# Optimization experiments

Hardware: AMD Instinct MI355X
Metric: run time of the kernel (lower is better)

## Reference

```python
import jax, jax.numpy as jnp
import numpy as np

DIM_IN, DIM_OUT, DIM_CTX = 128, 256, 259
B, N, S_CTX = 32, 2048, 1
BN_EPS = 1e-5


def setup_inputs() -> dict:
    key = jax.random.key(0)
    ks = jax.random.split(key, 12)
    s = 0.02
    return {
        "ctx": jax.random.normal(ks[0], (B, S_CTX, DIM_CTX), jnp.float32),
        "x": jax.random.normal(ks[1], (B, N, DIM_IN), jnp.float32),
        "W_layer": jax.random.normal(ks[2], (DIM_OUT, DIM_IN), jnp.float32) * s,
        "b_layer": jax.random.normal(ks[3], (DIM_OUT,), jnp.float32) * s,
        "W_hbias": jax.random.normal(ks[4], (DIM_OUT, DIM_CTX), jnp.float32) * s,
        "W_gate": jax.random.normal(ks[5], (DIM_OUT, DIM_CTX), jnp.float32) * s,
        "b_gate": jax.random.normal(ks[6], (DIM_OUT,), jnp.float32) * s,
        "W_k": jax.random.normal(ks[7], (DIM_OUT, DIM_CTX - 3), jnp.float32) * s,
        "W_v": jax.random.normal(ks[8], (DIM_OUT, DIM_CTX - 3), jnp.float32) * s,
        "W_tc": jax.random.normal(ks[9], (DIM_OUT, DIM_OUT), jnp.float32) * s,
        "b_tc": jax.random.normal(ks[10], (DIM_OUT,), jnp.float32) * s,
        "bn_gamma": jnp.ones((N,), jnp.float32),
        "bn_beta": jnp.zeros((N,), jnp.float32),
    }


def reference(ctx, x, W_layer, b_layer, W_hbias, W_gate, b_gate, W_k, W_v, W_tc, b_tc, bn_gamma, bn_beta):
    # FiLM gate / bias from context: [B, 1, dim_out]
    gate = jax.nn.sigmoid(jnp.einsum('bsc,oc->bso', ctx, W_gate) + b_gate)
    bias = jnp.einsum('bsc,oc->bso', ctx, W_hbias)

    # main linear: [B, N, dim_out]
    x1 = jnp.einsum('bni,oi->bno', x, W_layer) + b_layer

    # channel attention from shape context (drop last 3 ctx dims)
    shape = ctx[:, :, : ctx.shape[2] - 3]                      # [B, S, C-3]
    shape_k = jnp.einsum('bsc,oc->bos', shape, W_k)            # [B, dim_out, S]
    shape_v = jnp.einsum('bsc,oc->bso', shape, W_v)            # [B, S, dim_out]
    energy = jnp.einsum('bos,bse->boe', shape_k, shape_v)      # [B, dim_out, dim_out]
    attention = jax.nn.softmax(energy, axis=-1)
    attention = attention / (1e-9 + attention.sum(axis=1, keepdims=True))

    # channel mixing: [B, N, dim_out]
    x_r = jnp.einsum('bno,boe->bne', x1, attention)

    # trans_conv + BatchNorm1d(N) (train-mode batch stats over dims (0, 2)) + ReLU
    t = jnp.einsum('bno,eo->bne', x1 - x_r, W_tc) + b_tc       # [B, N, dim_out]
    mean = t.mean(axis=(0, 2), keepdims=True)                  # per point-channel
    var = t.var(axis=(0, 2), keepdims=True)                    # biased variance
    t = (t - mean) * jax.lax.rsqrt(var + BN_EPS)
    t = t * bn_gamma[None, :, None] + bn_beta[None, :, None]
    x_r = jax.nn.relu(t)

    xo = x1 + x_r
    return xo * gate + bias
```

## Files before the change

kernel.cpp:

```cpp
#include <hip/hip_runtime.h>
#include <hip/hip_bf16.h>

#define BB   32
#define NN   2048
#define DIN  128
#define DOUT 256
#define DCTX 259

#define OFF_TT   0u
#define OFF_AB   0u
#define OFF_MTB  1048576u
#define OFF_X1B  8388608u
#define OFF_WMB  16777216u
#define OFF_WLB  17301504u
#define OFF_WLTB 17317888u
#define OFF_WTCB 17334272u
#define OFF_G    17367040u
#define OFF_HB   17375232u
#define OFF_TB   17383424u
#define OFF_WKT  17391616u
#define OFF_WVT  17457152u
#define OFF_WGT  17522688u
#define OFF_WHT  17588992u

typedef short bf16x8 __attribute__((ext_vector_type(8)));
typedef float f32x4  __attribute__((ext_vector_type(4)));

static __device__ inline unsigned short f2bf(float f) {
    __hip_bfloat16 h = __float2bfloat16(f);
    return *(unsigned short*)&h;
}
static __device__ inline float bf2f(unsigned short u) {
    unsigned v = ((unsigned)u) << 16;
    float f;
    __builtin_memcpy(&f, &v, 4);
    return f;
}

__global__ void kXW(const float* __restrict__ Wl, const float* __restrict__ Wtc,
                    const float* __restrict__ Wk, const float* __restrict__ Wv,
                    const float* __restrict__ Wg, const float* __restrict__ Whb,
                    float* __restrict__ ws) {
    unsigned bb = blockIdx.x, t = threadIdx.x;
    if (bb < 8u) {
        unsigned base = bb * 8192u;
        unsigned short* dst = (unsigned short*)(ws + OFF_WTCB);
#pragma unroll
        for (int j = 0; j < 32; j++) {
            unsigned i = base + (unsigned)j * 256u + t;
            dst[i] = f2bf(Wtc[i]);
        }
    } else if (bb == 8u) {
        unsigned short* dst = (unsigned short*)(ws + OFF_WLTB);
        for (unsigned idx = t; idx < 32768u; idx += 256u) {
            unsigned i = idx >> 8, o = idx & 255u;
            dst[idx] = f2bf(Wl[o * 128u + i]);
        }
    } else if (bb == 9u) {
        unsigned short* dst = (unsigned short*)(ws + OFF_WLB);
        for (unsigned idx = t; idx < 32768u; idx += 256u) dst[idx] = f2bf(Wl[idx]);
    } else {
        unsigned j = bb - 10u;
        const float* src; float* dst; unsigned C, c0;
        if (j < 8u)       { src = Wk;  dst = ws + OFF_WKT; C = 256; c0 = j * 32u; }
        else if (j < 16u) { src = Wv;  dst = ws + OFF_WVT; C = 256; c0 = (j - 8u) * 32u; }
        else if (j < 25u) { src = Wg;  dst = ws + OFF_WGT; C = 259; c0 = (j - 16u) * 32u; }
        else              { src = Whb; dst = ws + OFF_WHT; C = 259; c0 = (j - 25u) * 32u; }
        for (unsigned cc = c0; cc < c0 + 32u && cc < C; cc++)
            dst[cc * 256u + t] = src[t * C + cc];
    }
}

__global__ __launch_bounds__(1024) void kP(const float* __restrict__ ctx,
                                           const float* __restrict__ bg,
                                           float* __restrict__ ws) {
    const int b = blockIdx.x, t = threadIdx.x;
    const int o = t & 255, q = t >> 8;
    __shared__ __align__(16) float cs[260];
    __shared__ __align__(16) float ks[256], vs[256], rms[256], ris[256];
    __shared__ float pm[1024], ps[1024];
    for (int i = t; i < DCTX; i += 1024) cs[i] = ctx[b * DCTX + i];
    __syncthreads();

    {
        const float* WT; int C;
        if (q == 0)      { WT = ws + OFF_WKT; C = 256; }
        else if (q == 1) { WT = ws + OFF_WVT; C = 256; }
        else if (q == 2) { WT = ws + OFF_WGT; C = DCTX; }
        else             { WT = ws + OFF_WHT; C = DCTX; }
        float s = 0.f;
#pragma unroll 8
        for (int c = 0; c < C; c++) s += WT[c * 256 + o] * cs[c];
        if (q == 0)      ks[o] = s;
        else if (q == 1) vs[o] = s;
        else if (q == 2) ws[OFF_G + b * DOUT + o] = 1.f / (1.f + __expf(-(s + bg[o])));
        else             ws[OFF_HB + b * DOUT + o] = s;
    }
    __syncthreads();

    const float ko = ks[o];
    const float4* vs4 = (const float4*)vs;
    float pmax = -1e30f;
#pragma unroll 4
    for (int j = q * 16; j < q * 16 + 16; j++) {
        float4 v = vs4[j];
        pmax = fmaxf(pmax, fmaxf(fmaxf(ko * v.x, ko * v.y), fmaxf(ko * v.z, ko * v.w)));
    }
    pm[q * 256 + o] = pmax;
    __syncthreads();
    float m = fmaxf(fmaxf(pm[o], pm[256 + o]), fmaxf(pm[512 + o], pm[768 + o]));
    float psum = 0.f;
#pragma unroll 4
    for (int j = q * 16; j < q * 16 + 16; j++) {
        float4 v = vs4[j];
        psum += __expf(ko * v.x - m) + __expf(ko * v.y - m)
              + __expf(ko * v.z - m) + __expf(ko * v.w - m);
    }
    ps[q * 256 + o] = psum;
    __syncthreads();
    float ri = 1.f / (ps[o] + ps[256 + o] + ps[512 + o] + ps[768 + o]);
    if (q == 0) { rms[o] = m; ris[o] = ri; }
    __syncthreads();

    const float ve = vs[o];
    float cp = 0.f;
#pragma unroll 4
    for (int o2 = q * 64; o2 < q * 64 + 64; o2++)
        cp += __expf(ks[o2] * ve - rms[o2]) * ris[o2];
    pm[q * 256 + o] = cp;
    __syncthreads();
    float ci = 1.f / (1e-9f + pm[o] + pm[256 + o] + pm[512 + o] + pm[768 + o]);
    unsigned short* Ab = (unsigned short*)(ws + OFF_AB) + (size_t)b * 65536u;
#pragma unroll 4
    for (int o2 = q * 64; o2 < q * 64 + 64; o2++) {
        float a = __expf(ks[o2] * ve - rms[o2]) * ris[o2] * ci;
        Ab[o2 * 256 + o] = f2bf(a);
    }
}

__global__ __launch_bounds__(256) void k4m(float* __restrict__ ws) {
    const int t = threadIdx.x, wid = t >> 6, l = t & 63;
    const int b = blockIdx.y, et = blockIdx.x;
    const int lrow = l & 15, lk = l >> 4;
    const int rbase = et * 64 + (wid & 1) * 32;
    const int colbase = (wid >> 1) * 128;
    const unsigned short* Wtcb = (const unsigned short*)(ws + OFF_WTCB);
    const unsigned short* Ab = (const unsigned short*)(ws + OFF_AB) + (size_t)b * 65536u;

    f32x4 acc[2][8];
#pragma unroll
    for (int i = 0; i < 2; i++)
#pragma unroll
        for (int c = 0; c < 8; c++) acc[i][c] = (f32x4){0.f, 0.f, 0.f, 0.f};

    const unsigned short* ar0 = Wtcb + (rbase + lrow) * 256;
#pragma unroll
    for (int kk = 0; kk < 8; kk++) {
        int ko = kk * 32 + lk * 8;
        bf16x8 a0 = *(const bf16x8*)(ar0 + ko);
        bf16x8 a1 = *(const bf16x8*)(ar0 + 16 * 256 + ko);
        bf16x8 bfr[8];
#pragma unroll
        for (int c = 0; c < 8; c++)
            bfr[c] = *(const bf16x8*)(Ab + (colbase + c * 16 + lrow) * 256 + ko);
#pragma unroll
        for (int c = 0; c < 8; c++) {
            acc[0][c] = __builtin_amdgcn_mfma_f32_16x16x32_bf16(a0, bfr[c], acc[0][c], 0, 0, 0);
            acc[1][c] = __builtin_amdgcn_mfma_f32_16x16x32_bf16(a1, bfr[c], acc[1][c], 0, 0, 0);
        }
    }
    unsigned short* Mtb = (unsigned short*)(ws + OFF_MTB) + (size_t)b * 65536u;
#pragma unroll
    for (int t2 = 0; t2 < 2; t2++)
#pragma unroll
        for (int c = 0; c < 8; c++)
#pragma unroll
            for (int r = 0; r < 4; r++) {
                int row = rbase + t2 * 16 + lk * 4 + r;
                int col = colbase + c * 16 + lrow;
                float idv = bf2f(Wtcb[row * 256 + col]);
                Mtb[row * 256 + col] = f2bf(idv - acc[t2][c][r]);
            }
}

__global__ __launch_bounds__(256) void k5m(const float* __restrict__ bl,
                                           const float* __restrict__ btc,
                                           float* __restrict__ ws) {
    const int t = threadIdx.x, wid = t >> 6, l = t & 63;
    const int b = blockIdx.y, et = blockIdx.x;
    const int lrow = l & 15, lk = l >> 4;
    const int rbase = et * 128 + wid * 32;
    const unsigned short* Mtb = (const unsigned short*)(ws + OFF_MTB) + (size_t)b * 65536u;
    const unsigned short* Wltb = (const unsigned short*)(ws + OFF_WLTB);

    f32x4 acc[2][8];
#pragma unroll
    for (int i = 0; i < 2; i++)
#pragma unroll
        for (int c = 0; c < 8; c++) acc[i][c] = (f32x4){0.f, 0.f, 0.f, 0.f};

    const unsigned short* ar0 = Mtb + (rbase + lrow) * 256;
#pragma unroll
    for (int kk = 0; kk < 8; kk++) {
        int ko = kk * 32 + lk * 8;
        bf16x8 a0 = *(const bf16x8*)(ar0 + ko);
        bf16x8 a1 = *(const bf16x8*)(ar0 + 16 * 256 + ko);
        bf16x8 bfr[8];
#pragma unroll
        for (int c = 0; c < 8; c++)
            bfr[c] = *(const bf16x8*)(Wltb + (c * 16 + lrow) * 256 + ko);
#pragma unroll
        for (int c = 0; c < 8; c++) {
            acc[0][c] = __builtin_amdgcn_mfma_f32_16x16x32_bf16(a0, bfr[c], acc[0][c], 0, 0, 0);
            acc[1][c] = __builtin_amdgcn_mfma_f32_16x16x32_bf16(a1, bfr[c], acc[1][c], 0, 0, 0);
        }
    }
    unsigned short* WMBp = (unsigned short*)(ws + OFF_WMB) + (size_t)b * 32768u;
#pragma unroll
    for (int t2 = 0; t2 < 2; t2++)
#pragma unroll
        for (int c = 0; c < 8; c++)
#pragma unroll
            for (int r = 0; r < 4; r++) {
                int row = rbase + t2 * 16 + lk * 4 + r;
                int col = c * 16 + lrow;
                WMBp[row * 128 + col] = f2bf(acc[t2][c][r]);
            }
    if (t < 128) {
        int e = et * 128 + t;
        const unsigned short* mrow = Mtb + e * 256;
        float s = 0.f;
#pragma unroll 8
        for (int o = 0; o < 256; o++) s += bl[o] * bf2f(mrow[o]);
        ws[OFF_TB + b * DOUT + e] = s + btc[e];
    }
}

#define LDP 136
__global__ __launch_bounds__(256) void k6_mfma(const float* __restrict__ x,
                                               const float* __restrict__ bl,
                                               float* __restrict__ ws) {
    const int t = threadIdx.x;
    const int wid = t >> 6, l = t & 63;
    const int b = blockIdx.y;
    const int n0 = blockIdx.x * 64;
    const int lrow = l & 15, lk = l >> 4;
    __shared__ unsigned short xs[64 * LDP];

    const float4* xg = (const float4*)(x + (size_t)(b * NN + n0) * DIN);
#pragma unroll
    for (int it = 0; it < 8; it++) {
        int idx = it * 256 + t;
        int row = idx >> 5, kq = idx & 31;
        float4 v = xg[idx];
        ushort4 u;
        u.x = f2bf(v.x); u.y = f2bf(v.y); u.z = f2bf(v.z); u.w = f2bf(v.w);
        *(ushort4*)(xs + row * LDP + kq * 4) = u;
    }
    __syncthreads();

    unsigned short* x1p = (unsigned short*)(ws + OFF_X1B);
    unsigned short* ttp = (unsigned short*)(ws + OFF_TT);
    const int colbase = wid * 64;

#pragma unroll
    for (int tc = 0; tc < 2; tc++) {
        const unsigned short* wb = (tc == 0)
            ? (const unsigned short*)(ws + OFF_WLB)
            : (const unsigned short*)(ws + OFF_WMB) + (size_t)b * 32768u;
        float bias[4];
#pragma unroll
        for (int ct = 0; ct < 4; ct++) {
            int col = colbase + ct * 16 + lrow;
            bias[ct] = (tc == 0) ? bl[col] : ws[OFF_TB + b * DOUT + col];
        }
        f32x4 acc[4][4];
#pragma unroll
        for (int rt = 0; rt < 4; rt++)
#pragma unroll
            for (int ct = 0; ct < 4; ct++) acc[rt][ct] = (f32x4){0.f, 0.f, 0.f, 0.f};

#pragma unroll
        for (int kk = 0; kk < 4; kk++) {
            int ko = kk * 32 + lk * 8;
            bf16x8 a[4];
#pragma unroll
            for (int rt = 0; rt < 4; rt++)
                a[rt] = *(const bf16x8*)(xs + (rt * 16 + lrow) * LDP + ko);
            bf16x8 bf[4];
#pragma unroll
            for (int ct = 0; ct < 4; ct++)
                bf[ct] = *(const bf16x8*)(wb + (size_t)(colbase + ct * 16 + lrow) * DIN + ko);
#pragma unroll
            for (int rt = 0; rt < 4; rt++)
#pragma unroll
                for (int ct = 0; ct < 4; ct++)
                    acc[rt][ct] = __builtin_amdgcn_mfma_f32_16x16x32_bf16(a[rt], bf[ct], acc[rt][ct], 0, 0, 0);
        }
        unsigned short* dst = (tc == 0) ? x1p : ttp;
#pragma unroll
        for (int rt = 0; rt < 4; rt++)
#pragma unroll
            for (int ct = 0; ct < 4; ct++)
#pragma unroll
                for (int r = 0; r < 4; r++) {
                    int row = n0 + rt * 16 + lk * 4 + r;
                    int col = colbase + ct * 16 + lrow;
                    dst[(size_t)((b * NN + row) * DOUT) + col] = f2bf(acc[rt][ct][r] + bias[ct]);
                }
    }
}

__global__ __launch_bounds__(1024) void k78(const float* __restrict__ gamma,
                                            const float* __restrict__ beta,
                                            float* __restrict__ out,
                                            float* __restrict__ ws) {
    const int n = blockIdx.x, t = threadIdx.x;
    const int o = t & 255, q = t >> 8;
    const int wid = t >> 6, l = t & 63;
    const unsigned short* ttb = (const unsigned short*)(ws + OFF_TT);
    const unsigned short* x1b = (const unsigned short*)(ws + OFF_X1B);
    float v[8];
    float s1 = 0.f, s2 = 0.f;
#pragma unroll
    for (int j = 0; j < 8; j++) {
        int b = q * 8 + j;
        float vv = bf2f(ttb[((size_t)b * NN + n) * DOUT + o]);
        v[j] = vv; s1 += vv; s2 += vv * vv;
    }
#pragma unroll
    for (int off = 32; off > 0; off >>= 1) {
        s1 += __shfl_xor(s1, off, 64);
        s2 += __shfl_xor(s2, off, 64);
    }
    __shared__ float p1[16], p2[16];
    if (l == 0) { p1[wid] = s1; p2[wid] = s2; }
    __syncthreads();
    float S1 = 0.f, S2 = 0.f;
#pragma unroll
    for (int w = 0; w < 16; w++) { S1 += p1[w]; S2 += p2[w]; }
    float mean = S1 * (1.f / 8192.f);
    float var  = S2 * (1.f / 8192.f) - mean * mean;
    float sc = gamma[n] * rsqrtf(fmaxf(var, 0.f) + 1e-5f);
    float sh = beta[n] - mean * sc;
#pragma unroll
    for (int j = 0; j < 8; j++) {
        int b = q * 8 + j;
        float x1 = bf2f(x1b[((size_t)b * NN + n) * DOUT + o]);
        float g  = ws[OFF_G  + b * DOUT + o];
        float hb = ws[OFF_HB + b * DOUT + o];
        out[((size_t)b * NN + n) * DOUT + o] = (x1 + fmaxf(v[j] * sc + sh, 0.f)) * g + hb;
    }
}

extern "C" void kernel_launch(void* const* d_in, const int* in_sizes, int n_in,
                              void* d_out, int out_size, void* d_ws, size_t ws_size,
                              hipStream_t stream) {
    const float* ctx   = (const float*)d_in[0];
    const float* x     = (const float*)d_in[1];
    const float* Wl    = (const float*)d_in[2];
    const float* bl    = (const float*)d_in[3];
    const float* Whb   = (const float*)d_in[4];
    const float* Wg    = (const float*)d_in[5];
    const float* bg    = (const float*)d_in[6];
    const float* Wk    = (const float*)d_in[7];
    const float* Wv    = (const float*)d_in[8];
    const float* Wtc   = (const float*)d_in[9];
    const float* btc   = (const float*)d_in[10];
    const float* gamma = (const float*)d_in[11];
    const float* beta  = (const float*)d_in[12];
    float* out = (float*)d_out;
    float* ws  = (float*)d_ws;

    kXW     <<<44, 256, 0, stream>>>(Wl, Wtc, Wk, Wv, Wg, Whb, ws);
    kP      <<<BB, 1024, 0, stream>>>(ctx, bg, ws);
    k4m     <<<dim3(4, BB), 256, 0, stream>>>(ws);
    k5m     <<<dim3(2, BB), 256, 0, stream>>>(bl, btc, ws);
    k6_mfma <<<dim3(32, BB), 256, 0, stream>>>(x, bl, ws);
    k78     <<<NN, 1024, 0, stream>>>(gamma, beta, out, ws);
}
```

Before: 240.4 us.

## Fuse the BN statistics pass into the GEMM with atomics and a per-tile spin barrier

Merges k4m and k5m into one kernel that keeps the intermediate M matrix in swizzled LDS rather than global memory. Merges the x1/t GEMM kernel with the BatchNorm+ReLU+FiLM epilogue. Per-point batch statistics are reduced with atomics, and the 32 batch blocks of each n-tile synchronise on a spin counter. This removes the bf16 t tensor round trip through HBM and two kernel launches. In exchange it needs all 1024 blocks to be co-resident, otherwise the spin barrier deadlocks, and atomic ordering makes the float sums nondeterministic.

```diff
diff --git a/kernel.cpp b/kernel.cpp
--- a/kernel.cpp
+++ b/kernel.cpp
@@ -9,7 +9,6 @@
 
 #define OFF_TT   0u
 #define OFF_AB   0u
-#define OFF_MTB  1048576u
 #define OFF_X1B  8388608u
 #define OFF_WMB  16777216u
 #define OFF_WLB  17301504u
@@ -22,6 +21,8 @@
 #define OFF_WVT  17457152u
 #define OFF_WGT  17522688u
 #define OFF_WHT  17588992u
+#define OFF_STATS 17655296u
+#define OFF_CNT   17659392u
 
 typedef short bf16x8 __attribute__((ext_vector_type(8)));
 typedef float f32x4  __attribute__((ext_vector_type(4)));
@@ -59,6 +60,8 @@
     } else if (bb == 9u) {
         unsigned short* dst = (unsigned short*)(ws + OFF_WLB);
         for (unsigned idx = t; idx < 32768u; idx += 256u) dst[idx] = f2bf(Wl[idx]);
+    } else if (bb == 44u) {
+        for (unsigned i = t; i < 4128u; i += 256u) ws[OFF_STATS + i] = 0.f;
     } else {
         unsigned j = bb - 10u;
         const float* src; float* dst; unsigned C, c0;
@@ -138,114 +141,115 @@
     }
 }
 
-__global__ __launch_bounds__(256) void k4m(float* __restrict__ ws) {
-    const int t = threadIdx.x, wid = t >> 6, l = t & 63;
-    const int b = blockIdx.y, et = blockIdx.x;
-    const int lrow = l & 15, lk = l >> 4;
-    const int rbase = et * 64 + (wid & 1) * 32;
-    const int colbase = (wid >> 1) * 128;
-    const unsigned short* Wtcb = (const unsigned short*)(ws + OFF_WTCB);
-    const unsigned short* Ab = (const unsigned short*)(ws + OFF_AB) + (size_t)b * 65536u;
-
-    f32x4 acc[2][8];
-#pragma unroll
-    for (int i = 0; i < 2; i++)
-#pragma unroll
-        for (int c = 0; c < 8; c++) acc[i][c] = (f32x4){0.f, 0.f, 0.f, 0.f};
-
-    const unsigned short* ar0 = Wtcb + (rbase + lrow) * 256;
-#pragma unroll
-    for (int kk = 0; kk < 8; kk++) {
-        int ko = kk * 32 + lk * 8;
-        bf16x8 a0 = *(const bf16x8*)(ar0 + ko);
-        bf16x8 a1 = *(const bf16x8*)(ar0 + 16 * 256 + ko);
-        bf16x8 bfr[8];
-#pragma unroll
-        for (int c = 0; c < 8; c++)
-            bfr[c] = *(const bf16x8*)(Ab + (colbase + c * 16 + lrow) * 256 + ko);
-#pragma unroll
-        for (int c = 0; c < 8; c++) {
-            acc[0][c] = __builtin_amdgcn_mfma_f32_16x16x32_bf16(a0, bfr[c], acc[0][c], 0, 0, 0);
-            acc[1][c] = __builtin_amdgcn_mfma_f32_16x16x32_bf16(a1, bfr[c], acc[1][c], 0, 0, 0);
-        }
-    }
-    unsigned short* Mtb = (unsigned short*)(ws + OFF_MTB) + (size_t)b * 65536u;
-#pragma unroll
-    for (int t2 = 0; t2 < 2; t2++)
-#pragma unroll
-        for (int c = 0; c < 8; c++)
-#pragma unroll
-            for (int r = 0; r < 4; r++) {
-                int row = rbase + t2 * 16 + lk * 4 + r;
-                int col = colbase + c * 16 + lrow;
-                float idv = bf2f(Wtcb[row * 256 + col]);
-                Mtb[row * 256 + col] = f2bf(idv - acc[t2][c][r]);
-            }
-}
-
-__global__ __launch_bounds__(256) void k5m(const float* __restrict__ bl,
+__global__ __launch_bounds__(512) void k45(const float* __restrict__ bl,
                                            const float* __restrict__ btc,
                                            float* __restrict__ ws) {
     const int t = threadIdx.x, wid = t >> 6, l = t & 63;
     const int b = blockIdx.y, et = blockIdx.x;
     const int lrow = l & 15, lk = l >> 4;
-    const int rbase = et * 128 + wid * 32;
-    const unsigned short* Mtb = (const unsigned short*)(ws + OFF_MTB) + (size_t)b * 65536u;
-    const unsigned short* Wltb = (const unsigned short*)(ws + OFF_WLTB);
-
-    f32x4 acc[2][8];
-#pragma unroll
-    for (int i = 0; i < 2; i++)
-#pragma unroll
-        for (int c = 0; c < 8; c++) acc[i][c] = (f32x4){0.f, 0.f, 0.f, 0.f};
-
-    const unsigned short* ar0 = Mtb + (rbase + lrow) * 256;
-#pragma unroll
-    for (int kk = 0; kk < 8; kk++) {
-        int ko = kk * 32 + lk * 8;
-        bf16x8 a0 = *(const bf16x8*)(ar0 + ko);
-        bf16x8 a1 = *(const bf16x8*)(ar0 + 16 * 256 + ko);
-        bf16x8 bfr[8];
+    __shared__ unsigned short Mt[128 * 256];
+    const unsigned short* Wtcb = (const unsigned short*)(ws + OFF_WTCB);
+
+    {
+        const unsigned short* Ab = (const unsigned short*)(ws + OFF_AB) + (size_t)b * 65536u;
+        const int sub = wid >> 2, w2 = wid & 3;
+        const int rbase = et * 128 + sub * 64 + (w2 & 1) * 32;
+        const int colbase = (w2 >> 1) * 128;
+        f32x4 acc[2][8];
+#pragma unroll
+        for (int i = 0; i < 2; i++)
+#pragma unroll
+            for (int c = 0; c < 8; c++) acc[i][c] = (f32x4){0.f, 0.f, 0.f, 0.f};
+        const unsigned short* ar0 = Wtcb + (rbase + lrow) * 256;
+#pragma unroll
+        for (int kk = 0; kk < 8; kk++) {
+            int ko = kk * 32 + lk * 8;
+            bf16x8 a0 = *(const bf16x8*)(ar0 + ko);
+            bf16x8 a1 = *(const bf16x8*)(ar0 + 16 * 256 + ko);
+            bf16x8 bfr[8];
+#pragma unroll
+            for (int c = 0; c < 8; c++)
+                bfr[c] = *(const bf16x8*)(Ab + (colbase + c * 16 + lrow) * 256 + ko);
+#pragma unroll
+            for (int c = 0; c < 8; c++) {
+                acc[0][c] = __builtin_amdgcn_mfma_f32_16x16x32_bf16(a0, bfr[c], acc[0][c], 0, 0, 0);
+                acc[1][c] = __builtin_amdgcn_mfma_f32_16x16x32_bf16(a1, bfr[c], acc[1][c], 0, 0, 0);
+            }
+        }
+#pragma unroll
+        for (int t2 = 0; t2 < 2; t2++)
+#pragma unroll
+            for (int c = 0; c < 8; c++)
+#pragma unroll
+                for (int r = 0; r < 4; r++) {
+                    int grow = rbase + t2 * 16 + lk * 4 + r;
+                    int col = colbase + c * 16 + lrow;
+                    float idv = bf2f(Wtcb[grow * 256 + col]);
+                    int rl = grow - et * 128;
+                    Mt[rl * 256 + (col ^ ((rl & 7) << 3))] = f2bf(idv - acc[t2][c][r]);
+                }
+    }
+    __syncthreads();
+    {
+        const unsigned short* Wltb = (const unsigned short*)(ws + OFF_WLTB);
+        const int rl0 = wid * 16;
+        f32x4 acc[8];
+#pragma unroll
+        for (int c = 0; c < 8; c++) acc[c] = (f32x4){0.f, 0.f, 0.f, 0.f};
+        const int arow = rl0 + lrow;
+        const int asw = (arow & 7) << 3;
+#pragma unroll
+        for (int kk = 0; kk < 8; kk++) {
+            int ko = kk * 32 + lk * 8;
+            bf16x8 a0 = *(const bf16x8*)(Mt + arow * 256 + (ko ^ asw));
+            bf16x8 bfr[8];
+#pragma unroll
+            for (int c = 0; c < 8; c++)
+                bfr[c] = *(const bf16x8*)(Wltb + (c * 16 + lrow) * 256 + ko);
+#pragma unroll
+            for (int c = 0; c < 8; c++)
+                acc[c] = __builtin_amdgcn_mfma_f32_16x16x32_bf16(a0, bfr[c], acc[c], 0, 0, 0);
+        }
+        unsigned short* WMBp = (unsigned short*)(ws + OFF_WMB) + (size_t)b * 32768u;
 #pragma unroll
         for (int c = 0; c < 8; c++)
-            bfr[c] = *(const bf16x8*)(Wltb + (c * 16 + lrow) * 256 + ko);
-#pragma unroll
-        for (int c = 0; c < 8; c++) {
-            acc[0][c] = __builtin_amdgcn_mfma_f32_16x16x32_bf16(a0, bfr[c], acc[0][c], 0, 0, 0);
-            acc[1][c] = __builtin_amdgcn_mfma_f32_16x16x32_bf16(a1, bfr[c], acc[1][c], 0, 0, 0);
-        }
-    }
-    unsigned short* WMBp = (unsigned short*)(ws + OFF_WMB) + (size_t)b * 32768u;
-#pragma unroll
-    for (int t2 = 0; t2 < 2; t2++)
-#pragma unroll
-        for (int c = 0; c < 8; c++)
 #pragma unroll
             for (int r = 0; r < 4; r++) {
-                int row = rbase + t2 * 16 + lk * 4 + r;
+                int row = et * 128 + rl0 + lk * 4 + r;
                 int col = c * 16 + lrow;
-                WMBp[row * 128 + col] = f2bf(acc[t2][c][r]);
-            }
+                WMBp[row * 128 + col] = f2bf(acc[c][r]);
+            }
+    }
     if (t < 128) {
-        int e = et * 128 + t;
-        const unsigned short* mrow = Mtb + e * 256;
+        const int rl = t;
+        const int sw = (rl & 7) << 3;
         float s = 0.f;
-#pragma unroll 8
-        for (int o = 0; o < 256; o++) s += bl[o] * bf2f(mrow[o]);
-        ws[OFF_TB + b * DOUT + e] = s + btc[e];
+#pragma unroll 4
+        for (int j = 0; j < 32; j++) {
+            bf16x8 ch = *(const bf16x8*)(Mt + rl * 256 + ((j * 8) ^ sw));
+#pragma unroll
+            for (int u = 0; u < 8; u++) s += bl[j * 8 + u] * bf2f((unsigned short)ch[u]);
+        }
+        ws[OFF_TB + b * DOUT + et * 128 + rl] = s + btc[et * 128 + rl];
     }
 }
 
 #define LDP 136
-__global__ __launch_bounds__(256) void k6_mfma(const float* __restrict__ x,
-                                               const float* __restrict__ bl,
-                                               float* __restrict__ ws) {
+__global__ __launch_bounds__(256, 4) void kF(const float* __restrict__ x,
+                                             const float* __restrict__ bl,
+                                             const float* __restrict__ gamma,
+                                             const float* __restrict__ beta,
+                                             float* __restrict__ out,
+                                             float* __restrict__ ws) {
     const int t = threadIdx.x;
     const int wid = t >> 6, l = t & 63;
     const int b = blockIdx.y;
-    const int n0 = blockIdx.x * 64;
+    const int nt = blockIdx.x;
+    const int n0 = nt * 64;
     const int lrow = l & 15, lk = l >> 4;
     __shared__ unsigned short xs[64 * LDP];
+    __shared__ float sp1[4][64], sp2[4][64];
+    __shared__ float scs[64], shs[64];
 
     const float4* xg = (const float4*)(x + (size_t)(b * NN + n0) * DIN);
 #pragma unroll
@@ -259,27 +263,16 @@
     }
     __syncthreads();
 
+    const int colbase = wid * 64;
     unsigned short* x1p = (unsigned short*)(ws + OFF_X1B);
-    unsigned short* ttp = (unsigned short*)(ws + OFF_TT);
-    const int colbase = wid * 64;
-
-#pragma unroll
-    for (int tc = 0; tc < 2; tc++) {
-        const unsigned short* wb = (tc == 0)
-            ? (const unsigned short*)(ws + OFF_WLB)
-            : (const unsigned short*)(ws + OFF_WMB) + (size_t)b * 32768u;
-        float bias[4];
-#pragma unroll
-        for (int ct = 0; ct < 4; ct++) {
-            int col = colbase + ct * 16 + lrow;
-            bias[ct] = (tc == 0) ? bl[col] : ws[OFF_TB + b * DOUT + col];
-        }
-        f32x4 acc[4][4];
+
+    {
+        const unsigned short* wb = (const unsigned short*)(ws + OFF_WLB);
+        f32x4 acc0[4][4];
 #pragma unroll
         for (int rt = 0; rt < 4; rt++)
 #pragma unroll
-            for (int ct = 0; ct < 4; ct++) acc[rt][ct] = (f32x4){0.f, 0.f, 0.f, 0.f};
-
+            for (int ct = 0; ct < 4; ct++) acc0[rt][ct] = (f32x4){0.f, 0.f, 0.f, 0.f};
 #pragma unroll
         for (int kk = 0; kk < 4; kk++) {
             int ko = kk * 32 + lk * 8;
@@ -295,62 +288,139 @@
             for (int rt = 0; rt < 4; rt++)
 #pragma unroll
                 for (int ct = 0; ct < 4; ct++)
-                    acc[rt][ct] = __builtin_amdgcn_mfma_f32_16x16x32_bf16(a[rt], bf[ct], acc[rt][ct], 0, 0, 0);
-        }
-        unsigned short* dst = (tc == 0) ? x1p : ttp;
-#pragma unroll
-        for (int rt = 0; rt < 4; rt++)
-#pragma unroll
-            for (int ct = 0; ct < 4; ct++)
+                    acc0[rt][ct] = __builtin_amdgcn_mfma_f32_16x16x32_bf16(a[rt], bf[ct], acc0[rt][ct], 0, 0, 0);
+        }
+#pragma unroll
+        for (int ct = 0; ct < 4; ct++) {
+            float bv = bl[colbase + ct * 16 + lrow];
+#pragma unroll
+            for (int rt = 0; rt < 4; rt++)
 #pragma unroll
                 for (int r = 0; r < 4; r++) {
                     int row = n0 + rt * 16 + lk * 4 + r;
                     int col = colbase + ct * 16 + lrow;
-                    dst[(size_t)((b * NN + row) * DOUT) + col] = f2bf(acc[rt][ct][r] + bias[ct]);
+                    x1p[(size_t)((b * NN + row) * DOUT) + col] = f2bf(acc0[rt][ct][r] + bv);
                 }
-    }
-}
-
-__global__ __launch_bounds__(1024) void k78(const float* __restrict__ gamma,
-                                            const float* __restrict__ beta,
-                                            float* __restrict__ out,
-                                            float* __restrict__ ws) {
-    const int n = blockIdx.x, t = threadIdx.x;
-    const int o = t & 255, q = t >> 8;
-    const int wid = t >> 6, l = t & 63;
-    const unsigned short* ttb = (const unsigned short*)(ws + OFF_TT);
-    const unsigned short* x1b = (const unsigned short*)(ws + OFF_X1B);
-    float v[8];
-    float s1 = 0.f, s2 = 0.f;
-#pragma unroll
-    for (int j = 0; j < 8; j++) {
-        int b = q * 8 + j;
-        float vv = bf2f(ttb[((size_t)b * NN + n) * DOUT + o]);
-        v[j] = vv; s1 += vv; s2 += vv * vv;
-    }
-#pragma unroll
-    for (int off = 32; off > 0; off >>= 1) {
-        s1 += __shfl_xor(s1, off, 64);
-        s2 += __shfl_xor(s2, off, 64);
-    }
-    __shared__ float p1[16], p2[16];
-    if (l == 0) { p1[wid] = s1; p2[wid] = s2; }
-    __syncthreads();
-    float S1 = 0.f, S2 = 0.f;
-#pragma unroll
-    for (int w = 0; w < 16; w++) { S1 += p1[w]; S2 += p2[w]; }
-    float mean = S1 * (1.f / 8192.f);
-    float var  = S2 * (1.f / 8192.f) - mean * mean;
-    float sc = gamma[n] * rsqrtf(fmaxf(var, 0.f) + 1e-5f);
-    float sh = beta[n] - mean * sc;
-#pragma unroll
-    for (int j = 0; j < 8; j++) {
-        int b = q * 8 + j;
-        float x1 = bf2f(x1b[((size_t)b * NN + n) * DOUT + o]);
-        float g  = ws[OFF_G  + b * DOUT + o];
-        float hb = ws[OFF_HB + b * DOUT + o];
-        out[((size_t)b * NN + n) * DOUT + o] = (x1 + fmaxf(v[j] * sc + sh, 0.f)) * g + hb;
-    }
+        }
+    }
+
+    f32x4 acc[4][4];
+#pragma unroll
+    for (int rt = 0; rt < 4; rt++)
+#pragma unroll
+        for (int ct = 0; ct < 4; ct++) acc[rt][ct] = (f32x4){0.f, 0.f, 0.f, 0.f};
+    {
+        const unsigned short* wb = (const unsigned short*)(ws + OFF_WMB) + (size_t)b * 32768u;
+#pragma unroll
+        for (int kk = 0; kk < 4; kk++) {
+            int ko = kk * 32 + lk * 8;
+            bf16x8 a[4];
+#pragma unroll
+            for (int rt = 0; rt < 4; rt++)
+                a[rt] = *(const bf16x8*)(xs + (rt * 16 + lrow) * LDP + ko);
+            bf16x8 bf[4];
+#pragma unroll
+            for (int ct = 0; ct < 4; ct++)
+                bf[ct] = *(const bf16x8*)(wb + (size_t)(colbase + ct * 16 + lrow) * DIN + ko);
+#pragma unroll
+            for (int rt = 0; rt < 4; rt++)
+#pragma unroll
+                for (int ct = 0; ct < 4; ct++)
+                    acc[rt][ct] = __builtin_amdgcn_mfma_f32_16x16x32_bf16(a[rt], bf[ct], acc[rt][ct], 0, 0, 0);
+        }
+#pragma unroll
+        for (int ct = 0; ct < 4; ct++) {
+            float bv = ws[OFF_TB + b * DOUT + colbase + ct * 16 + lrow];
+#pragma unroll
+            for (int rt = 0; rt < 4; rt++)
+#pragma unroll
+                for (int r = 0; r < 4; r++) acc[rt][ct][r] += bv;
+        }
+    }
+
+    float s1[4][4], s2[4][4];
+#pragma unroll
+    for (int rt = 0; rt < 4; rt++)
+#pragma unroll
+        for (int r = 0; r < 4; r++) { s1[rt][r] = 0.f; s2[rt][r] = 0.f; }
+#pragma unroll
+    for (int rt = 0; rt < 4; rt++)
+#pragma unroll
+        for (int ct = 0; ct < 4; ct++)
+#pragma unroll
+            for (int r = 0; r < 4; r++) {
+                float v = acc[rt][ct][r];
+                s1[rt][r] += v; s2[rt][r] += v * v;
+            }
+#pragma unroll
+    for (int off = 1; off < 16; off <<= 1) {
+#pragma unroll
+        for (int rt = 0; rt < 4; rt++)
+#pragma unroll
+            for (int r = 0; r < 4; r++) {
+                s1[rt][r] += __shfl_xor(s1[rt][r], off, 64);
+                s2[rt][r] += __shfl_xor(s2[rt][r], off, 64);
+            }
+    }
+    if (lrow == 0) {
+#pragma unroll
+        for (int rt = 0; rt < 4; rt++)
+#pragma unroll
+            for (int r = 0; r < 4; r++) {
+                int nidx = rt * 16 + lk * 4 + r;
+                sp1[wid][nidx] = s1[rt][r];
+                sp2[wid][nidx] = s2[rt][r];
+            }
+    }
+    __syncthreads();
+    float* stats = ws + OFF_STATS;
+    if (t < 64) {
+        float S1 = sp1[0][t] + sp1[1][t] + sp1[2][t] + sp1[3][t];
+        float S2 = sp2[0][t] + sp2[1][t] + sp2[2][t] + sp2[3][t];
+        atomicAdd(stats + (size_t)(n0 + t) * 2, S1);
+        atomicAdd(stats + (size_t)(n0 + t) * 2 + 1, S2);
+    }
+    __syncthreads();
+
+    unsigned* cnt = (unsigned*)(ws + OFF_CNT) + nt;
+    if (t == 0) { __threadfence(); atomicAdd(cnt, 1u); }
+    while (__hip_atomic_load(cnt, __ATOMIC_RELAXED, __HIP_MEMORY_SCOPE_AGENT) < (unsigned)BB)
+        __builtin_amdgcn_s_sleep(8);
+    __threadfence();
+
+    if (t < 64) {
+        int n = n0 + t;
+        float S1 = stats[(size_t)n * 2], S2 = stats[(size_t)n * 2 + 1];
+        float mean = S1 * (1.f / 8192.f);
+        float var  = S2 * (1.f / 8192.f) - mean * mean;
+        float sc = gamma[n] * rsqrtf(fmaxf(var, 0.f) + 1e-5f);
+        scs[t] = sc;
+        shs[t] = beta[n] - mean * sc;
+    }
+    __syncthreads();
+
+    float gv[4], hbv[4];
+#pragma unroll
+    for (int ct = 0; ct < 4; ct++) {
+        int o = colbase + ct * 16 + lrow;
+        gv[ct]  = ws[OFF_G  + b * DOUT + o];
+        hbv[ct] = ws[OFF_HB + b * DOUT + o];
+    }
+#pragma unroll
+    for (int rt = 0; rt < 4; rt++)
+#pragma unroll
+        for (int r = 0; r < 4; r++) {
+            int nidx = rt * 16 + lk * 4 + r;
+            float sc = scs[nidx], sh = shs[nidx];
+            int n = n0 + nidx;
+#pragma unroll
+            for (int ct = 0; ct < 4; ct++) {
+                int o = colbase + ct * 16 + lrow;
+                float x1v = bf2f(x1p[(size_t)((b * NN + n) * DOUT) + o]);
+                float rv = fmaxf(acc[rt][ct][r] * sc + sh, 0.f);
+                out[(size_t)((b * NN + n) * DOUT) + o] = (x1v + rv) * gv[ct] + hbv[ct];
+            }
+        }
 }
 
 extern "C" void kernel_launch(void* const* d_in, const int* in_sizes, int n_in,
@@ -372,10 +442,8 @@
     float* out = (float*)d_out;
     float* ws  = (float*)d_ws;
 
-    kXW     <<<44, 256, 0, stream>>>(Wl, Wtc, Wk, Wv, Wg, Whb, ws);
-    kP      <<<BB, 1024, 0, stream>>>(ctx, bg, ws);
-    k4m     <<<dim3(4, BB), 256, 0, stream>>>(ws);
-    k5m     <<<dim3(2, BB), 256, 0, stream>>>(bl, btc, ws);
-    k6_mfma <<<dim3(32, BB), 256, 0, stream>>>(x, bl, ws);
-    k78     <<<NN, 1024, 0, stream>>>(gamma, beta, out, ws);
-}
+    kXW <<<45, 256, 0, stream>>>(Wl, Wtc, Wk, Wv, Wg, Whb, ws);
+    kP  <<<BB, 1024, 0, stream>>>(ctx, bg, ws);
+    k45 <<<dim3(2, BB), 512, 0, stream>>>(bl, btc, ws);
+    kF  <<<dim3(32, BB), 256, 0, stream>>>(x, bl, gamma, beta, out, ws);
+}
```

New measurement: 428.8 us. 78.4% more time.
